# Optimization experiments

Hardware: AMD Instinct MI355X
Metric: run time of the kernel (lower is better)

The kernel has to match this reference:

```python
import jax, jax.numpy as jnp
import numpy as np
from jax import lax

K_GROUPS = 4
CH = 256
CG = CH // K_GROUPS  # 64
KK = 9  # 3x3 kernel taps


def setup_inputs() -> dict:
    key = jax.random.key(0)
    ks = jax.random.split(key, 4)
    x = jax.random.normal(ks[0], (16, CH, 64, 64), dtype=jnp.float32)
    # offset-predicting conv: Cg -> 18 (2 offsets per 3x3 tap); small init so offsets are modest
    off_w = jax.random.normal(ks[1], (K_GROUPS, 18, CG, 3, 3), dtype=jnp.float32) * 0.01
    off_b = jnp.zeros((K_GROUPS, 18), dtype=jnp.float32)
    # deformable conv weights: Cg -> Cg, 3x3
    def_w = jax.random.normal(ks[2], (K_GROUPS, CG, CG, 3, 3), dtype=jnp.float32) * (1.0 / np.sqrt(CG * KK))
    def_b = jnp.zeros((K_GROUPS, CG), dtype=jnp.float32)
    return {"x": x, "off_w": off_w, "off_b": off_b, "def_w": def_w, "def_b": def_b}


def _bilinear_sample(img, py, px):
    # img: [B,Cg,H,W]; py,px: [B,KK,H,W] float sample coords -> [B,Cg,KK,H,W]
    B, C, H, W = img.shape
    K = py.shape[1]
    imgf = img.reshape(B, C, H * W)
    y0 = jnp.floor(py)
    x0 = jnp.floor(px)
    wy = py - y0
    wx = px - x0

    def gather(yi, xi, wgt):
        valid = (yi >= 0) & (yi < H) & (xi >= 0) & (xi < W)  # zero padding outside
        yc = jnp.clip(yi, 0, H - 1).astype(jnp.int32)
        xc = jnp.clip(xi, 0, W - 1).astype(jnp.int32)
        idx = (yc * W + xc).reshape(B, 1, K * H * W)
        v = jnp.take_along_axis(imgf, idx, axis=2).reshape(B, C, K, H, W)
        w = (wgt * valid.astype(img.dtype)).reshape(B, 1, K, H, W)
        return v * w

    return (gather(y0, x0, (1 - wy) * (1 - wx))
            + gather(y0, x0 + 1, (1 - wy) * wx)
            + gather(y0 + 1, x0, wy * (1 - wx))
            + gather(y0 + 1, x0 + 1, wy * wx))


def _group_forward(xg, ow, ob, dw, db):
    # xg: [B,Cg,H,W]
    B, C, H, W = xg.shape
    offset = lax.conv_general_dilated(xg, ow, (1, 1), ((1, 1), (1, 1)),
                                      dimension_numbers=("NCHW", "OIHW", "NCHW"))
    offset = offset + ob[None, :, None, None]            # [B,18,H,W]
    off = offset.reshape(B, KK, 2, H, W)                  # per-tap (dy,dx)
    ky, kx = jnp.meshgrid(jnp.arange(-1, 2), jnp.arange(-1, 2), indexing="ij")
    ky = ky.reshape(KK).astype(xg.dtype)
    kx = kx.reshape(KK).astype(xg.dtype)
    hh = jnp.arange(H, dtype=xg.dtype)
    ww = jnp.arange(W, dtype=xg.dtype)
    py = off[:, :, 0] + ky[None, :, None, None] + hh[None, None, :, None]  # [B,KK,H,W]
    px = off[:, :, 1] + kx[None, :, None, None] + ww[None, None, None, :]
    sampled = _bilinear_sample(xg, py, px)                # [B,Cg,KK,H,W]
    out = jnp.einsum("oik,bikhw->bohw", dw.reshape(dw.shape[0], dw.shape[1], KK), sampled)
    return out + db[None, :, None, None]


def reference(x, off_w, off_b, def_w, def_b):
    xs = jnp.split(x, K_GROUPS, axis=1)  # mirrors torch.split over channel groups
    outs = [_group_forward(xs[g], off_w[g], off_b[g], def_w[g], def_b[g])
            for g in range(K_GROUPS)]
    return jnp.concatenate(outs, axis=1)
```

## Files before the change

kernel.cpp:

```cpp
#include <hip/hip_runtime.h>
#include <hip/hip_bf16.h>
#include <hip/hip_fp16.h>

#define B_  16
#define G_  4
#define CG  64
#define H_  64
#define W_  64
#define KK  9
#define HW  (H_ * W_)
#define IP  72
#define PD  68
#define XSLICE (PD * PD * CG)

typedef short    short8  __attribute__((ext_vector_type(8)));
typedef _Float16 half8   __attribute__((ext_vector_type(8)));
typedef _Float16 h2      __attribute__((ext_vector_type(2)));
typedef float    f32x4   __attribute__((ext_vector_type(4)));
typedef float    f32x16  __attribute__((ext_vector_type(16)));

__device__ __forceinline__ short f2h(float v) {
    _Float16 h = (_Float16)v;
    short s;
    __builtin_memcpy(&s, &h, 2);
    return s;
}

__device__ __forceinline__ unsigned int pk2h(float a, float b) {
    h2 h = { (_Float16)a, (_Float16)b };
    unsigned int u;
    __builtin_memcpy(&u, &h, 4);
    return u;
}

__device__ __forceinline__ unsigned int interp2h(unsigned int c00, unsigned int c01,
                                                 unsigned int c10, unsigned int c11,
                                                 h2 w00, h2 w01, h2 w10, h2 w11) {
    h2 v00, v01, v10, v11;
    __builtin_memcpy(&v00, &c00, 4);
    __builtin_memcpy(&v01, &c01, 4);
    __builtin_memcpy(&v10, &c10, 4);
    __builtin_memcpy(&v11, &c11, 4);
    h2 r = v00 * w00 + v01 * w01 + v10 * w10 + v11 * w11;
    unsigned int o;
    __builtin_memcpy(&o, &r, 4);
    return o;
}

__global__ __launch_bounds__(256)
void prep_all(const float* __restrict__ x,
              const float* __restrict__ off_w,
              const float* __restrict__ def_w,
              short* __restrict__ xTpad,
              short* __restrict__ dwA32,
              short* __restrict__ owA)
{
    const int blk = blockIdx.x;
    const int t   = threadIdx.x;

    if (blk < 1024) {
        const int bg = blk >> 4;
        const int y0 = (blk & 15) * 4;

        __shared__ unsigned int sBw[4 * CG * 33];

        const float* src = x + (size_t)bg * CG * HW + (size_t)y0 * W_;
        const int i  = t >> 2;
        const int x0 = (t & 3) * 16;

        float4 v[4][4];
#pragma unroll
        for (int r = 0; r < 4; r++) {
            const float* sp = src + (size_t)i * HW + r * W_ + x0;
#pragma unroll
            for (int c = 0; c < 4; c++) v[r][c] = ((const float4*)sp)[c];
        }

#pragma unroll
        for (int r = 0; r < 4; r++) {
#pragma unroll
            for (int c = 0; c < 4; c++) {
                const unsigned int u0 = pk2h(v[r][c].x, v[r][c].y);
                const unsigned int u1 = pk2h(v[r][c].z, v[r][c].w);
                const int base = (r * CG + i) * 33 + ((x0 + 4 * c) >> 1);
                sBw[base]     = u0;
                sBw[base + 1] = u1;
            }
        }
        __syncthreads();

        const short* sBs = (const short*)sBw;
        short* dst = xTpad + (size_t)bg * XSLICE;
#pragma unroll
        for (int r = 0; r < 4; r++) {
            const int yp = y0 + 2 + r;
            for (int task = t; task < PD * 8; task += 256) {
                const int ich = task & 7;
                const int xp  = task >> 3;
                const int xx  = xp - 2;
                short8 o = {0, 0, 0, 0, 0, 0, 0, 0};
                if ((unsigned)xx < (unsigned)W_) {
#pragma unroll
                    for (int e = 0; e < 8; e++)
                        o[e] = sBs[(r * CG + ich * 8 + e) * 66 + xx];
                }
                *(short8*)(dst + ((size_t)yp * PD + xp) * CG + ich * 8) = o;
            }
        }
        return;
    }

    if (blk < 1088) {
        const int bg = blk - 1024;
        short* dstb = xTpad + (size_t)bg * XSLICE;
        const int4 z = {0, 0, 0, 0};
        int4* d0 = (int4*)(dstb);
        int4* d1 = (int4*)(dstb + (size_t)66 * PD * CG);
        const int n16 = (2 * PD * CG * 2) / 16;
        for (int c = t; c < n16; c += 256) { d0[c] = z; d1[c] = z; }
        return;
    }

    const int tid = (blk - 1088) * 256 + t;
    const int ndw = G_ * KK * 4096;
    const int now = G_ * 18 * 2 * 4 * 16 * 8;
    if (tid < ndw) {
        const int e    = tid & 7;
        const int o    = (tid >> 3) & 31;
        const int q2   = (tid >> 8) & 1;
        const int step = (tid >> 9) & 3;
        const int mt   = (tid >> 11) & 1;
        const int gk   = tid >> 12;
        const int k    = gk % KK;
        const int g    = gk / KK;
        const int oo   = mt * 32 + o;
        const int i    = step * 16 + q2 * 8 + e;
        dwA32[tid] = f2h(def_w[((g * CG + oo) * CG + i) * KK + k]);
    } else if (tid < ndw + now) {
        const int t2 = tid - ndw;
        const int e  = t2 & 7;
        const int jj = (t2 >> 3) & 15;
        const int q  = (t2 >> 7) & 3;
        const int tm = (t2 >> 9) & 1;
        const int gs = t2 >> 10;
        const int s  = gs % 18;
        const int g  = gs / 18;
        const int j  = tm * 16 + jj;
        const int rc = s >> 1;
        const int i  = (s & 1) * 32 + q * 8 + e;
        owA[t2] = (j < 18) ? f2h(off_w[((g * 18 + j) * CG + i) * KK + rc]) : (short)0;
    }
}

__global__ __launch_bounds__(256, 7)
void deform_main(const short* __restrict__ xTpad,
                 const float* __restrict__ off_b,
                 const float* __restrict__ def_b,
                 const short* __restrict__ dwA32,
                 const short* __restrict__ owA,
                 float* __restrict__ out)
{
    const int raw = blockIdx.x;
    const int r8  = raw & 7;
    const int h   = (raw >> 3) & 63;
    const int q8  = raw >> 9;
    const int bg  = q8 * 8 + r8;
    const int b   = bg >> 2;
    const int g   = bg & 3;

    __shared__ float2 pcs[KK][64];
    __shared__ short  sT[2][64 * IP];

    const int t    = threadIdx.x;
    const int lane = t & 63;
    const int p    = t >> 6;
    const int nn   = lane & 15;
    const int q    = lane >> 4;

    const short* xb = xTpad + (size_t)bg * XSLICE;

    {
        const short* owAg = owA + g * 18 * 1024;
        f32x4 oa0 = {0.f, 0.f, 0.f, 0.f};
        f32x4 oa1 = {0.f, 0.f, 0.f, 0.f};
#pragma unroll
        for (int rc = 0; rc < 9; rc++) {
            const int rr = rc / 3;
            const int cc = rc % 3;
            const short* cp = xb + ((h + rr + 1) * PD + (p * 16 + nn + cc + 1)) * CG + q * 8;
            const half8 b0 = *(const half8*)cp;
            const half8 b1 = *(const half8*)(cp + 32);
            const int s0 = rc * 2, s1 = rc * 2 + 1;
            const half8 a00 = *(const half8*)(owAg + ((s0 * 2 + 0) * 4 + q) * 128 + nn * 8);
            const half8 a01 = *(const half8*)(owAg + ((s0 * 2 + 1) * 4 + q) * 128 + nn * 8);
            const half8 a10 = *(const half8*)(owAg + ((s1 * 2 + 0) * 4 + q) * 128 + nn * 8);
            const half8 a11 = *(const half8*)(owAg + ((s1 * 2 + 1) * 4 + q) * 128 + nn * 8);
            oa0 = __builtin_amdgcn_mfma_f32_16x16x32_f16(a00, b0, oa0, 0, 0, 0);
            oa1 = __builtin_amdgcn_mfma_f32_16x16x32_f16(a01, b0, oa1, 0, 0, 0);
            oa0 = __builtin_amdgcn_mfma_f32_16x16x32_f16(a10, b1, oa0, 0, 0, 0);
            oa1 = __builtin_amdgcn_mfma_f32_16x16x32_f16(a11, b1, oa1, 0, 0, 0);
        }
        const int n = p * 16 + nn;
#pragma unroll
        for (int reg = 0; reg < 4; reg++) {
            const int j  = q * 4 + reg;
            const int kk = j >> 1;
            const float v = oa0[reg] + off_b[g * 18 + j];
            if ((j & 1) == 0) pcs[kk][n].x = v + (float)(kk / 3) + (float)(h + 1);
            else              pcs[kk][n].y = v + (float)(kk % 3) + (float)(n + 1);
        }
        if (q == 0) {
            pcs[8][n].x = oa1[0] + off_b[g * 18 + 16] + 2.0f + (float)(h + 1);
            pcs[8][n].y = oa1[1] + off_b[g * 18 + 17] + 2.0f + (float)(n + 1);
        }
    }

    const int mt  = p >> 1;
    const int nt  = p & 1;
    const int n31 = lane & 31;
    const int q2  = lane >> 5;

    f32x16 acc = {0.f};
    const short* dwg = dwA32 + g * KK * 4096;

    const int posL  = lane >> 3;
    const int chidx = lane & 7;

    auto gather_tap = [&](int k, short* __restrict__ sTb) {
#pragma unroll
        for (int it = 0; it < 2; it++) {
            const int pos = p * 16 + it * 8 + posL;
            const float2 pc = pcs[k][pos];
            const float yf = floorf(pc.x);
            const float xf = floorf(pc.y);
            const float wy = pc.x - yf;
            const float wx = pc.y - xf;
            int y0 = (int)yf;
            int x0 = (int)xf;
            y0 = (y0 < 0) ? 0 : ((y0 > 66) ? 66 : y0);
            x0 = (x0 < 0) ? 0 : ((x0 > 66) ? 66 : x0);
            const short* cp = xb + (y0 * PD + x0) * CG + chidx * 8;
            const uint4 c00 = *(const uint4*)cp;
            const uint4 c01 = *(const uint4*)(cp + CG);
            const uint4 c10 = *(const uint4*)(cp + PD * CG);
            const uint4 c11 = *(const uint4*)(cp + PD * CG + CG);
            const float a00 = (1.0f - wy) * (1.0f - wx);
            const float a01 = (1.0f - wy) * wx;
            const float a10 = wy * (1.0f - wx);
            const float a11 = wy * wx;
            const h2 w00 = { (_Float16)a00, (_Float16)a00 };
            const h2 w01 = { (_Float16)a01, (_Float16)a01 };
            const h2 w10 = { (_Float16)a10, (_Float16)a10 };
            const h2 w11 = { (_Float16)a11, (_Float16)a11 };
            uint4 ov;
            ov.x = interp2h(c00.x, c01.x, c10.x, c11.x, w00, w01, w10, w11);
            ov.y = interp2h(c00.y, c01.y, c10.y, c11.y, w00, w01, w10, w11);
            ov.z = interp2h(c00.z, c01.z, c10.z, c11.z, w00, w01, w10, w11);
            ov.w = interp2h(c00.w, c01.w, c10.w, c11.w, w00, w01, w10, w11);
            *(uint4*)&sTb[pos * IP + chidx * 8] = ov;
        }
    };

    auto einsum_tap = [&](int k, const short* __restrict__ sTb) {
        const short* dwk = dwg + k * 4096;
#pragma unroll
        for (int step = 0; step < 4; step++) {
            const half8 af = *(const half8*)(dwk + ((mt * 4 + step) * 2 + q2) * 256 + n31 * 8);
            const half8 bf = *(const half8*)&sTb[(nt * 32 + n31) * IP + step * 16 + q2 * 8];
            acc = __builtin_amdgcn_mfma_f32_32x32x16_f16(af, bf, acc, 0, 0, 0);
        }
    };

    gather_tap(0, &sT[0][0]);
    __syncthreads();
    for (int k = 0; k < KK; k++) {
        if (k < KK - 1) gather_tap(k + 1, &sT[(k + 1) & 1][0]);
        einsum_tap(k, &sT[k & 1][0]);
        __syncthreads();
    }

    float* outb = out + (size_t)(b * 256 + g * 64) * HW + h * W_;
    const int n = nt * 32 + n31;
#pragma unroll
    for (int reg = 0; reg < 16; reg++) {
        const int o = mt * 32 + (reg & 3) + 8 * (reg >> 2) + 4 * q2;
        outb[(size_t)o * HW + n] = acc[reg] + def_b[g * 64 + o];
    }
}

__global__ __launch_bounds__(256, 4)
void deform_fallback(const float* __restrict__ x,
                     const float* __restrict__ off_w,
                     const float* __restrict__ off_b,
                     const float* __restrict__ def_w,
                     const float* __restrict__ def_b,
                     float* __restrict__ out)
{
    const int raw = blockIdx.x;
    const int r8  = raw & 7;
    const int h   = (raw >> 3) & 63;
    const int q8  = raw >> 9;
    const int bg  = q8 * 8 + r8;
    const int b   = bg >> 2;
    const int g   = bg & 3;

    __shared__ float pys[KK][W_];
    __shared__ float pxs[KK][W_];
    __shared__ float buf[8192];
    float* red   = buf;
    float* s_lds = buf;
    float* dwTl  = buf + 4096;

    const int t = threadIdx.x;
    const int w = t & 63;
    const int p = t >> 6;

    const float* xg = x + (size_t)(b * 256 + g * 64) * HW;

    float acc[18];
#pragma unroll
    for (int j = 0; j < 18; j++) acc[j] = 0.0f;
    {
        const int i0 = p * 16;
        for (int ii = 0; ii < 16; ii++) {
            const int i = i0 + ii;
            const float* xi = xg + i * HW;
#pragma unroll
            for (int r = 0; r < 3; r++) {
                const int y = h + r - 1;
                if ((unsigned)y >= (unsigned)H_) continue;
#pragma unroll
                for (int c = 0; c < 3; c++) {
                    const int xc = w + c - 1;
                    const float xv = ((unsigned)xc < (unsigned)W_) ? xi[y * W_ + xc] : 0.0f;
#pragma unroll
                    for (int j = 0; j < 18; j++) {
                        const float wv = off_w[((g * 18 + j) * CG + i) * 9 + r * 3 + c];
                        acc[j] = fmaf(wv, xv, acc[j]);
                    }
                }
            }
        }
    }
#pragma unroll
    for (int j = 0; j < 18; j++) red[(p * 18 + j) * 64 + w] = acc[j];
    __syncthreads();
    for (int idx = t; idx < 18 * 64; idx += 256) {
        const int j  = idx >> 6;
        const int ww = idx & 63;
        float v = red[(0 * 18 + j) * 64 + ww] + red[(1 * 18 + j) * 64 + ww]
                + red[(2 * 18 + j) * 64 + ww] + red[(3 * 18 + j) * 64 + ww];
        v += off_b[g * 18 + j];
        const int k = j >> 1;
        if ((j & 1) == 0) pys[k][ww] = v + (float)(k / 3 - 1) + (float)h;
        else              pxs[k][ww] = v + (float)(k % 3 - 1) + (float)ww;
    }
    __syncthreads();

    float facc[16];
#pragma unroll
    for (int qd = 0; qd < 16; qd++) facc[qd] = 0.0f;
    const int w4 = (t & 15) << 2;
    const int o4 = (t >> 4) << 2;

    for (int k = 0; k < KK; k++) {
#pragma unroll
        for (int n = 0; n < 16; n++) {
            const int v = t + 256 * n;
            const int i = v >> 6;
            const int o = v & 63;
            dwTl[v] = def_w[((g * CG + o) * CG + i) * KK + k];
        }
        const float py  = pys[k][w];
        const float px  = pxs[k][w];
        const float y0f = floorf(py);
        const float x0f = floorf(px);
        const float wy  = py - y0f;
        const float wx  = px - x0f;
        const int   y0  = (int)y0f;
        const int   x0  = (int)x0f;
        const float w00 = (1.0f - wy) * (1.0f - wx);
        const float w01 = (1.0f - wy) * wx;
        const float w10 = wy * (1.0f - wx);
        const float w11 = wy * wx;
        const bool vy0 = (unsigned)y0       < (unsigned)H_;
        const bool vy1 = (unsigned)(y0 + 1) < (unsigned)H_;
        const bool vx0 = (unsigned)x0       < (unsigned)W_;
        const bool vx1 = (unsigned)(x0 + 1) < (unsigned)W_;
        const int a00 = y0 * W_ + x0;
#pragma unroll
        for (int n = 0; n < 16; n++) {
            const int i = (n << 2) + p;
            const float* xi = xg + i * HW;
            const float v00 = (vy0 && vx0) ? xi[a00]          : 0.0f;
            const float v01 = (vy0 && vx1) ? xi[a00 + 1]      : 0.0f;
            const float v10 = (vy1 && vx0) ? xi[a00 + W_]     : 0.0f;
            const float v11 = (vy1 && vx1) ? xi[a00 + W_ + 1] : 0.0f;
            s_lds[i * 64 + w] = w00 * v00 + w01 * v01 + w10 * v10 + w11 * v11;
        }
        __syncthreads();
#pragma unroll 4
        for (int i = 0; i < CG; i++) {
            const float4 sv = *(const float4*)&s_lds[i * 64 + w4];
            const float4 dv = *(const float4*)&dwTl[i * 64 + o4];
            facc[0]  = fmaf(dv.x, sv.x, facc[0]);
            facc[1]  = fmaf(dv.x, sv.y, facc[1]);
            facc[2]  = fmaf(dv.x, sv.z, facc[2]);
            facc[3]  = fmaf(dv.x, sv.w, facc[3]);
            facc[4]  = fmaf(dv.y, sv.x, facc[4]);
            facc[5]  = fmaf(dv.y, sv.y, facc[5]);
            facc[6]  = fmaf(dv.y, sv.z, facc[6]);
            facc[7]  = fmaf(dv.y, sv.w, facc[7]);
            facc[8]  = fmaf(dv.z, sv.x, facc[8]);
            facc[9]  = fmaf(dv.z, sv.y, facc[9]);
            facc[10] = fmaf(dv.z, sv.z, facc[10]);
            facc[11] = fmaf(dv.z, sv.w, facc[11]);
            facc[12] = fmaf(dv.w, sv.x, facc[12]);
            facc[13] = fmaf(dv.w, sv.y, facc[13]);
            facc[14] = fmaf(dv.w, sv.z, facc[14]);
            facc[15] = fmaf(dv.w, sv.w, facc[15]);
        }
        __syncthreads();
    }

    float* outp = out + (size_t)(b * 256 + g * 64) * HW + h * W_;
#pragma unroll
    for (int oo = 0; oo < 4; oo++) {
        const int o = o4 + oo;
        const float bias = def_b[g * 64 + o];
        float4 r;
        r.x = facc[oo * 4 + 0] + bias;
        r.y = facc[oo * 4 + 1] + bias;
        r.z = facc[oo * 4 + 2] + bias;
        r.w = facc[oo * 4 + 3] + bias;
        *(float4*)&outp[o * HW + w4] = r;
    }
}

extern "C" void kernel_launch(void* const* d_in, const int* in_sizes, int n_in,
                              void* d_out, int out_size, void* d_ws, size_t ws_size,
                              hipStream_t stream)
{
    (void)in_sizes; (void)n_in; (void)out_size;
    const float* x     = (const float*)d_in[0];
    const float* off_w = (const float*)d_in[1];
    const float* off_b = (const float*)d_in[2];
    const float* def_w = (const float*)d_in[3];
    const float* def_b = (const float*)d_in[4];
    float* out = (float*)d_out;

    const size_t xT_bytes  = (size_t)B_ * G_ * XSLICE * 2;
    const size_t dw_bytes  = (size_t)G_ * KK * 4096 * 2;
    const size_t ow_bytes  = (size_t)G_ * 18 * 1024 * 2;
    const size_t need = xT_bytes + dw_bytes + ow_bytes;

    const int nblk   = B_ * G_ * H_;
    const int nprepw = (G_ * KK * 4096 + G_ * 18 * 1024 + 255) / 256;
    const int nprep  = 1024 + 64 + nprepw;

    if (ws_size >= need) {
        short* xTpad = (short*)d_ws;
        short* dwA32 = (short*)((char*)d_ws + xT_bytes);
        short* owA   = (short*)((char*)d_ws + xT_bytes + dw_bytes);
        prep_all<<<nprep, 256, 0, stream>>>(x, off_w, def_w, xTpad, dwA32, owA);
        deform_main<<<nblk, 256, 0, stream>>>(xTpad, off_b, def_b, dwA32, owA, out);
    } else {
        deform_fallback<<<nblk, 256, 0, stream>>>(x, off_w, off_b, def_w, def_b, out);
    }
}
```

Baseline: 221.0 us.

## Make each wave own its pixel slice to drop block barriers in tap loop

Restructures the einsum so each wave computes all 64 output channels for its own 16 pixels with 16x16x32 MFMAs, instead of 32x32 tiles that share gathered data across waves. Each wave therefore only reads the samples it gathered itself, so the per-tap __syncthreads are removed and every wave gets private double-buffered LDS. Gather loads are split into issue and write phases kept in registers, so the next tap's global loads overlap the current MFMAs. The def_w prep layout changes to match, and launch bounds drop from 7 to 5 blocks per CU to make room for the extra registers, which lowers occupancy.

```diff
diff --git a/kernel.cpp b/kernel.cpp
--- a/kernel.cpp
+++ b/kernel.cpp
@@ -52,7 +52,7 @@
               const float* __restrict__ off_w,
               const float* __restrict__ def_w,
               short* __restrict__ xTpad,
-              short* __restrict__ dwA32,
+              short* __restrict__ dwA16,
               short* __restrict__ owA)
 {
     const int blk = blockIdx.x;
@@ -125,17 +125,16 @@
     const int ndw = G_ * KK * 4096;
     const int now = G_ * 18 * 2 * 4 * 16 * 8;
     if (tid < ndw) {
-        const int e    = tid & 7;
-        const int o    = (tid >> 3) & 31;
-        const int q2   = (tid >> 8) & 1;
-        const int step = (tid >> 9) & 3;
-        const int mt   = (tid >> 11) & 1;
-        const int gk   = tid >> 12;
-        const int k    = gk % KK;
-        const int g    = gk / KK;
-        const int oo   = mt * 32 + o;
-        const int i    = step * 16 + q2 * 8 + e;
-        dwA32[tid] = f2h(def_w[((g * CG + oo) * CG + i) * KK + k]);
+        const int e  = tid & 7;
+        const int l  = (tid >> 3) & 63;
+        const int kh = (tid >> 9) & 1;
+        const int ot = (tid >> 10) & 3;
+        const int gk = tid >> 12;
+        const int k  = gk % KK;
+        const int g  = gk / KK;
+        const int o  = ot * 16 + (l & 15);
+        const int i  = kh * 32 + (l >> 4) * 8 + e;
+        dwA16[tid] = f2h(def_w[((g * CG + o) * CG + i) * KK + k]);
     } else if (tid < ndw + now) {
         const int t2 = tid - ndw;
         const int e  = t2 & 7;
@@ -152,11 +151,11 @@
     }
 }
 
-__global__ __launch_bounds__(256, 7)
+__global__ __launch_bounds__(256, 5)
 void deform_main(const short* __restrict__ xTpad,
                  const float* __restrict__ off_b,
                  const float* __restrict__ def_b,
-                 const short* __restrict__ dwA32,
+                 const short* __restrict__ dwA16,
                  const short* __restrict__ owA,
                  float* __restrict__ out)
 {
@@ -169,7 +168,7 @@
     const int g   = bg & 3;
 
     __shared__ float2 pcs[KK][64];
-    __shared__ short  sT[2][64 * IP];
+    __shared__ short  sT[4][2][16 * IP];
 
     const int t    = threadIdx.x;
     const int lane = t & 63;
@@ -215,35 +214,40 @@
         }
     }
 
-    const int mt  = p >> 1;
-    const int nt  = p & 1;
-    const int n31 = lane & 31;
-    const int q2  = lane >> 5;
-
-    f32x16 acc = {0.f};
-    const short* dwg = dwA32 + g * KK * 4096;
-
     const int posL  = lane >> 3;
     const int chidx = lane & 7;
 
-    auto gather_tap = [&](int k, short* __restrict__ sTb) {
+    short* sW0 = &sT[p][0][0];
+    short* sW1 = &sT[p][1][0];
+
+    f32x4 acc[4] = { {0.f}, {0.f}, {0.f}, {0.f} };
+    const short* dwg = dwA16 + g * KK * 4096;
+
+    auto issue_tap = [&](int k, uint4* cr, float2* wv) {
 #pragma unroll
         for (int it = 0; it < 2; it++) {
             const int pos = p * 16 + it * 8 + posL;
             const float2 pc = pcs[k][pos];
             const float yf = floorf(pc.x);
             const float xf = floorf(pc.y);
-            const float wy = pc.x - yf;
-            const float wx = pc.y - xf;
+            wv[it] = make_float2(pc.x - yf, pc.y - xf);
             int y0 = (int)yf;
             int x0 = (int)xf;
             y0 = (y0 < 0) ? 0 : ((y0 > 66) ? 66 : y0);
             x0 = (x0 < 0) ? 0 : ((x0 > 66) ? 66 : x0);
             const short* cp = xb + (y0 * PD + x0) * CG + chidx * 8;
-            const uint4 c00 = *(const uint4*)cp;
-            const uint4 c01 = *(const uint4*)(cp + CG);
-            const uint4 c10 = *(const uint4*)(cp + PD * CG);
-            const uint4 c11 = *(const uint4*)(cp + PD * CG + CG);
+            cr[it * 4 + 0] = *(const uint4*)cp;
+            cr[it * 4 + 1] = *(const uint4*)(cp + CG);
+            cr[it * 4 + 2] = *(const uint4*)(cp + PD * CG);
+            cr[it * 4 + 3] = *(const uint4*)(cp + PD * CG + CG);
+        }
+    };
+
+    auto write_tap = [&](short* __restrict__ sTb, const uint4* cr, const float2* wv) {
+#pragma unroll
+        for (int it = 0; it < 2; it++) {
+            const float wy = wv[it].x;
+            const float wx = wv[it].y;
             const float a00 = (1.0f - wy) * (1.0f - wx);
             const float a01 = (1.0f - wy) * wx;
             const float a10 = wy * (1.0f - wx);
@@ -252,39 +256,57 @@
             const h2 w01 = { (_Float16)a01, (_Float16)a01 };
             const h2 w10 = { (_Float16)a10, (_Float16)a10 };
             const h2 w11 = { (_Float16)a11, (_Float16)a11 };
+            const uint4 c00 = cr[it * 4 + 0];
+            const uint4 c01 = cr[it * 4 + 1];
+            const uint4 c10 = cr[it * 4 + 2];
+            const uint4 c11 = cr[it * 4 + 3];
             uint4 ov;
             ov.x = interp2h(c00.x, c01.x, c10.x, c11.x, w00, w01, w10, w11);
             ov.y = interp2h(c00.y, c01.y, c10.y, c11.y, w00, w01, w10, w11);
             ov.z = interp2h(c00.z, c01.z, c10.z, c11.z, w00, w01, w10, w11);
             ov.w = interp2h(c00.w, c01.w, c10.w, c11.w, w00, w01, w10, w11);
-            *(uint4*)&sTb[pos * IP + chidx * 8] = ov;
+            *(uint4*)&sTb[(it * 8 + posL) * IP + chidx * 8] = ov;
         }
     };
 
     auto einsum_tap = [&](int k, const short* __restrict__ sTb) {
         const short* dwk = dwg + k * 4096;
 #pragma unroll
-        for (int step = 0; step < 4; step++) {
-            const half8 af = *(const half8*)(dwk + ((mt * 4 + step) * 2 + q2) * 256 + n31 * 8);
-            const half8 bf = *(const half8*)&sTb[(nt * 32 + n31) * IP + step * 16 + q2 * 8];
-            acc = __builtin_amdgcn_mfma_f32_32x32x16_f16(af, bf, acc, 0, 0, 0);
+        for (int kh = 0; kh < 2; kh++) {
+            const half8 bf = *(const half8*)&sTb[nn * IP + kh * 32 + q * 8];
+#pragma unroll
+            for (int ot = 0; ot < 4; ot++) {
+                const half8 af = *(const half8*)(dwk + ((ot * 2 + kh) * 64 + lane) * 8);
+                acc[ot] = __builtin_amdgcn_mfma_f32_16x16x32_f16(af, bf, acc[ot], 0, 0, 0);
+            }
         }
     };
 
-    gather_tap(0, &sT[0][0]);
-    __syncthreads();
+    uint4  crA[8], crB[8];
+    float2 wvA[2], wvB[2];
+
+    issue_tap(0, crA, wvA);
+    write_tap(sW0, crA, wvA);
+#pragma unroll
     for (int k = 0; k < KK; k++) {
-        if (k < KK - 1) gather_tap(k + 1, &sT[(k + 1) & 1][0]);
-        einsum_tap(k, &sT[k & 1][0]);
-        __syncthreads();
+        short*  bufCur = ((k & 1) == 0) ? sW0 : sW1;
+        short*  bufNxt = ((k & 1) == 0) ? sW1 : sW0;
+        uint4*  crN    = ((k & 1) == 0) ? crB : crA;
+        float2* wvN    = ((k & 1) == 0) ? wvB : wvA;
+        if (k < KK - 1) issue_tap(k + 1, crN, wvN);
+        einsum_tap(k, bufCur);
+        if (k < KK - 1) write_tap(bufNxt, crN, wvN);
     }
 
     float* outb = out + (size_t)(b * 256 + g * 64) * HW + h * W_;
-    const int n = nt * 32 + n31;
-#pragma unroll
-    for (int reg = 0; reg < 16; reg++) {
-        const int o = mt * 32 + (reg & 3) + 8 * (reg >> 2) + 4 * q2;
-        outb[(size_t)o * HW + n] = acc[reg] + def_b[g * 64 + o];
+    const int n = p * 16 + nn;
+#pragma unroll
+    for (int ot = 0; ot < 4; ot++) {
+#pragma unroll
+        for (int reg = 0; reg < 4; reg++) {
+            const int o = ot * 16 + q * 4 + reg;
+            outb[(size_t)o * HW + n] = acc[ot][reg] + def_b[g * 64 + o];
+        }
     }
 }
 
@@ -460,10 +482,10 @@
 
     if (ws_size >= need) {
         short* xTpad = (short*)d_ws;
-        short* dwA32 = (short*)((char*)d_ws + xT_bytes);
+        short* dwA16 = (short*)((char*)d_ws + xT_bytes);
         short* owA   = (short*)((char*)d_ws + xT_bytes + dw_bytes);
-        prep_all<<<nprep, 256, 0, stream>>>(x, off_w, def_w, xTpad, dwA32, owA);
-        deform_main<<<nblk, 256, 0, stream>>>(xTpad, off_b, def_b, dwA32, owA, out);
+        prep_all<<<nprep, 256, 0, stream>>>(x, off_w, def_w, xTpad, dwA16, owA);
+        deform_main<<<nblk, 256, 0, stream>>>(xTpad, off_b, def_b, dwA16, owA, out);
     } else {
         deform_fallback<<<nblk, 256, 0, stream>>>(x, off_w, off_b, def_w, def_b, out);
     }
```

After: 234.6 us. 1.06x slower.

## Stage 5-row input window in XOR-swizzled LDS for offset conv and gather

Applied to the files above, without the earlier changes.

Each block now loads a 5-row by 66-column window of the padded fp16 input into shared memory, with an XOR swizzle to avoid bank conflicts. The offset-prediction conv reads its B operands from this window, and the bilinear gather reads its four corners from it when the sample falls inside. Out-of-window samples still read from global memory. The extra LDS footprint (about 42 KB) leads to lowering launch_bounds occupancy from 7 to 2. This trades global/L2 traffic for lower occupancy and a load phase followed by a barrier.

```diff
diff --git a/kernel.cpp b/kernel.cpp
--- a/kernel.cpp
+++ b/kernel.cpp
@@ -12,6 +12,11 @@
 #define IP  72
 #define PD  68
 #define XSLICE (PD * PD * CG)
+
+#define WROWS 5
+#define WCOLS 66
+#define NCELL (WROWS * WCOLS)
+#define NSLOT (NCELL * 8)
 
 typedef short    short8  __attribute__((ext_vector_type(8)));
 typedef _Float16 half8   __attribute__((ext_vector_type(8)));
@@ -152,7 +157,7 @@
     }
 }
 
-__global__ __launch_bounds__(256, 7)
+__global__ __launch_bounds__(256, 2)
 void deform_main(const short* __restrict__ xTpad,
                  const float* __restrict__ off_b,
                  const float* __restrict__ def_b,
@@ -168,6 +173,7 @@
     const int b   = bg >> 2;
     const int g   = bg & 3;
 
+    __shared__ short  sX[NSLOT * 8];
     __shared__ float2 pcs[KK][64];
     __shared__ short  sT[2][64 * IP];
 
@@ -180,6 +186,32 @@
     const short* xb = xTpad + (size_t)bg * XSLICE;
 
     {
+        uint4 tmp[10];
+#pragma unroll
+        for (int j = 0; j < 10; j++) {
+            const int s    = j * 256 + t;
+            const int cell = s >> 3;
+            const int c    = (s & 7) ^ (cell & 7);
+            const int rr   = cell / WCOLS;
+            const int colx = 1 + (cell - rr * WCOLS);
+            tmp[j] = *(const uint4*)(xb + ((h + rr) * PD + colx) * CG + c * 8);
+        }
+        uint4 tl;
+        const int st = 2560 + t;
+        if (t < NSLOT - 2560) {
+            const int cell = st >> 3;
+            const int c    = (st & 7) ^ (cell & 7);
+            const int rr   = cell / WCOLS;
+            const int colx = 1 + (cell - rr * WCOLS);
+            tl = *(const uint4*)(xb + ((h + rr) * PD + colx) * CG + c * 8);
+        }
+#pragma unroll
+        for (int j = 0; j < 10; j++) *(uint4*)&sX[(j * 256 + t) * 8] = tmp[j];
+        if (t < NSLOT - 2560) *(uint4*)&sX[st * 8] = tl;
+    }
+    __syncthreads();
+
+    {
         const short* owAg = owA + g * 18 * 1024;
         f32x4 oa0 = {0.f, 0.f, 0.f, 0.f};
         f32x4 oa1 = {0.f, 0.f, 0.f, 0.f};
@@ -187,9 +219,10 @@
         for (int rc = 0; rc < 9; rc++) {
             const int rr = rc / 3;
             const int cc = rc % 3;
-            const short* cp = xb + ((h + rr + 1) * PD + (p * 16 + nn + cc + 1)) * CG + q * 8;
-            const half8 b0 = *(const half8*)cp;
-            const half8 b1 = *(const half8*)(cp + 32);
+            const int cA   = p * 16 + nn + cc + 1;
+            const int cell = (rr + 1) * WCOLS + (cA - 1);
+            const half8 b0 = *(const half8*)&sX[(cell * 8 + ( q      ^ (cell & 7))) * 8];
+            const half8 b1 = *(const half8*)&sX[(cell * 8 + ((q + 4) ^ (cell & 7))) * 8];
             const int s0 = rc * 2, s1 = rc * 2 + 1;
             const half8 a00 = *(const half8*)(owAg + ((s0 * 2 + 0) * 4 + q) * 128 + nn * 8);
             const half8 a01 = *(const half8*)(owAg + ((s0 * 2 + 1) * 4 + q) * 128 + nn * 8);
@@ -239,15 +272,32 @@
             int x0 = (int)xf;
             y0 = (y0 < 0) ? 0 : ((y0 > 66) ? 66 : y0);
             x0 = (x0 < 0) ? 0 : ((x0 > 66) ? 66 : x0);
-            const short* cp = xb + (y0 * PD + x0) * CG + chidx * 8;
-            const uint4 c00 = *(const uint4*)cp;
-            const uint4 c01 = *(const uint4*)(cp + CG);
-            const uint4 c10 = *(const uint4*)(cp + PD * CG);
-            const uint4 c11 = *(const uint4*)(cp + PD * CG + CG);
-            const float a00 = (1.0f - wy) * (1.0f - wx);
-            const float a01 = (1.0f - wy) * wx;
-            const float a10 = wy * (1.0f - wx);
-            const float a11 = wy * wx;
+            float a00 = (1.0f - wy) * (1.0f - wx);
+            float a01 = (1.0f - wy) * wx;
+            float a10 = wy * (1.0f - wx);
+            float a11 = wy * wx;
+            uint4 c00, c01, c10, c11;
+            const int ry = y0 - h;
+            if (ry >= 0 && ry <= WROWS - 2) {
+                int col0 = x0 - 1;
+                int col1 = x0;
+                if (col0 < 0)          { a00 = 0.f; a10 = 0.f; col0 = 0; }
+                if (col1 > WCOLS - 1)  { a01 = 0.f; a11 = 0.f; col1 = WCOLS - 1; }
+                const int ca = ry * WCOLS + col0;
+                const int cb = ry * WCOLS + col1;
+                const int cc_ = ca + WCOLS;
+                const int cd = cb + WCOLS;
+                c00 = *(const uint4*)&sX[(ca  * 8 + (chidx ^ (ca  & 7))) * 8];
+                c01 = *(const uint4*)&sX[(cb  * 8 + (chidx ^ (cb  & 7))) * 8];
+                c10 = *(const uint4*)&sX[(cc_ * 8 + (chidx ^ (cc_ & 7))) * 8];
+                c11 = *(const uint4*)&sX[(cd  * 8 + (chidx ^ (cd  & 7))) * 8];
+            } else {
+                const short* cp = xb + (y0 * PD + x0) * CG + chidx * 8;
+                c00 = *(const uint4*)cp;
+                c01 = *(const uint4*)(cp + CG);
+                c10 = *(const uint4*)(cp + PD * CG);
+                c11 = *(const uint4*)(cp + PD * CG + CG);
+            }
             const h2 w00 = { (_Float16)a00, (_Float16)a00 };
             const h2 w01 = { (_Float16)a01, (_Float16)a01 };
             const h2 w10 = { (_Float16)a10, (_Float16)a10 };
```

After: 232.9 us. 1.05x slower.

## Stage a 5-row input window in LDS and gather bilinear taps from it

Applied to the files above, without the earlier changes.

Each block now loads a 5x68-cell fp16 window of the padded input into shared memory. Both the offset-conv fragments and the bilinear corner reads come from LDS whenever the sample row falls inside the window, with a global-memory fallback otherwise. The double-buffered sT pipeline is replaced by a single buffer with two barriers per tap, and the next tap's deformable weights are prefetched into registers. The much larger LDS footprint (about 54KB) and the lower launch-bounds occupancy target (7 to 2 blocks) trade latency hiding for on-chip reuse.

```diff
diff --git a/kernel.cpp b/kernel.cpp
--- a/kernel.cpp
+++ b/kernel.cpp
@@ -12,6 +12,11 @@
 #define IP  72
 #define PD  68
 #define XSLICE (PD * PD * CG)
+
+#define WR   5
+#define WC   68
+#define CELLW 72
+#define NSLOT (WR * WC * 8)
 
 typedef short    short8  __attribute__((ext_vector_type(8)));
 typedef _Float16 half8   __attribute__((ext_vector_type(8)));
@@ -152,7 +157,7 @@
     }
 }
 
-__global__ __launch_bounds__(256, 7)
+__global__ __launch_bounds__(256, 2)
 void deform_main(const short* __restrict__ xTpad,
                  const float* __restrict__ off_b,
                  const float* __restrict__ def_b,
@@ -168,8 +173,9 @@
     const int b   = bg >> 2;
     const int g   = bg & 3;
 
+    __shared__ short  sX[WR * WC * CELLW];
+    __shared__ short  sT[64 * IP];
     __shared__ float2 pcs[KK][64];
-    __shared__ short  sT[2][64 * IP];
 
     const int t    = threadIdx.x;
     const int lane = t & 63;
@@ -180,6 +186,40 @@
     const short* xb = xTpad + (size_t)bg * XSLICE;
 
     {
+        uint4 tv[10];
+#pragma unroll
+        for (int j = 0; j < 10; j++) {
+            const int s    = j * 256 + t;
+            const int cell = s >> 3;
+            const int ch   = s & 7;
+            const int r    = cell / WC;
+            const int c    = cell - r * WC;
+            tv[j] = *(const uint4*)(xb + ((h + r) * PD + c) * CG + ch * 8);
+        }
+        uint4 tl;
+        if (t < NSLOT - 2560) {
+            const int s    = 2560 + t;
+            const int cell = s >> 3;
+            const int ch   = s & 7;
+            const int r    = cell / WC;
+            const int c    = cell - r * WC;
+            tl = *(const uint4*)(xb + ((h + r) * PD + c) * CG + ch * 8);
+        }
+#pragma unroll
+        for (int j = 0; j < 10; j++) {
+            const int s    = j * 256 + t;
+            const int cell = s >> 3;
+            const int ch   = s & 7;
+            *(uint4*)&sX[cell * CELLW + ch * 8] = tv[j];
+        }
+        if (t < NSLOT - 2560) {
+            const int s    = 2560 + t;
+            *(uint4*)&sX[(s >> 3) * CELLW + (s & 7) * 8] = tl;
+        }
+    }
+    __syncthreads();
+
+    {
         const short* owAg = owA + g * 18 * 1024;
         f32x4 oa0 = {0.f, 0.f, 0.f, 0.f};
         f32x4 oa1 = {0.f, 0.f, 0.f, 0.f};
@@ -187,9 +227,10 @@
         for (int rc = 0; rc < 9; rc++) {
             const int rr = rc / 3;
             const int cc = rc % 3;
-            const short* cp = xb + ((h + rr + 1) * PD + (p * 16 + nn + cc + 1)) * CG + q * 8;
-            const half8 b0 = *(const half8*)cp;
-            const half8 b1 = *(const half8*)(cp + 32);
+            const int cA   = p * 16 + nn + cc + 1;
+            const int cell = (rr + 1) * WC + cA;
+            const half8 b0 = *(const half8*)&sX[cell * CELLW + q * 8];
+            const half8 b1 = *(const half8*)&sX[cell * CELLW + (q + 4) * 8];
             const int s0 = rc * 2, s1 = rc * 2 + 1;
             const half8 a00 = *(const half8*)(owAg + ((s0 * 2 + 0) * 4 + q) * 128 + nn * 8);
             const half8 a01 = *(const half8*)(owAg + ((s0 * 2 + 1) * 4 + q) * 128 + nn * 8);
@@ -226,7 +267,7 @@
     const int posL  = lane >> 3;
     const int chidx = lane & 7;
 
-    auto gather_tap = [&](int k, short* __restrict__ sTb) {
+    auto gather_tap = [&](int k) {
 #pragma unroll
         for (int it = 0; it < 2; it++) {
             const int pos = p * 16 + it * 8 + posL;
@@ -239,11 +280,21 @@
             int x0 = (int)xf;
             y0 = (y0 < 0) ? 0 : ((y0 > 66) ? 66 : y0);
             x0 = (x0 < 0) ? 0 : ((x0 > 66) ? 66 : x0);
-            const short* cp = xb + (y0 * PD + x0) * CG + chidx * 8;
-            const uint4 c00 = *(const uint4*)cp;
-            const uint4 c01 = *(const uint4*)(cp + CG);
-            const uint4 c10 = *(const uint4*)(cp + PD * CG);
-            const uint4 c11 = *(const uint4*)(cp + PD * CG + CG);
+            uint4 c00, c01, c10, c11;
+            const int ry = y0 - h;
+            if ((unsigned)ry <= 3u) {
+                const int base = (ry * WC + x0) * CELLW + chidx * 8;
+                c00 = *(const uint4*)&sX[base];
+                c01 = *(const uint4*)&sX[base + CELLW];
+                c10 = *(const uint4*)&sX[base + WC * CELLW];
+                c11 = *(const uint4*)&sX[base + WC * CELLW + CELLW];
+            } else {
+                const short* cp = xb + (y0 * PD + x0) * CG + chidx * 8;
+                c00 = *(const uint4*)cp;
+                c01 = *(const uint4*)(cp + CG);
+                c10 = *(const uint4*)(cp + PD * CG);
+                c11 = *(const uint4*)(cp + PD * CG + CG);
+            }
             const float a00 = (1.0f - wy) * (1.0f - wx);
             const float a01 = (1.0f - wy) * wx;
             const float a10 = wy * (1.0f - wx);
@@ -257,25 +308,38 @@
             ov.y = interp2h(c00.y, c01.y, c10.y, c11.y, w00, w01, w10, w11);
             ov.z = interp2h(c00.z, c01.z, c10.z, c11.z, w00, w01, w10, w11);
             ov.w = interp2h(c00.w, c01.w, c10.w, c11.w, w00, w01, w10, w11);
-            *(uint4*)&sTb[pos * IP + chidx * 8] = ov;
+            *(uint4*)&sT[pos * IP + chidx * 8] = ov;
         }
     };
 
-    auto einsum_tap = [&](int k, const short* __restrict__ sTb) {
-        const short* dwk = dwg + k * 4096;
-#pragma unroll
-        for (int step = 0; step < 4; step++) {
-            const half8 af = *(const half8*)(dwk + ((mt * 4 + step) * 2 + q2) * 256 + n31 * 8);
-            const half8 bf = *(const half8*)&sTb[(nt * 32 + n31) * IP + step * 16 + q2 * 8];
-            acc = __builtin_amdgcn_mfma_f32_32x32x16_f16(af, bf, acc, 0, 0, 0);
-        }
-    };
-
-    gather_tap(0, &sT[0][0]);
-    __syncthreads();
+    half8 af0, af1, af2, af3, an0, an1, an2, an3;
+    {
+        const short* dwk = dwg;
+        af0 = *(const half8*)(dwk + ((mt * 4 + 0) * 2 + q2) * 256 + n31 * 8);
+        af1 = *(const half8*)(dwk + ((mt * 4 + 1) * 2 + q2) * 256 + n31 * 8);
+        af2 = *(const half8*)(dwk + ((mt * 4 + 2) * 2 + q2) * 256 + n31 * 8);
+        af3 = *(const half8*)(dwk + ((mt * 4 + 3) * 2 + q2) * 256 + n31 * 8);
+    }
+
     for (int k = 0; k < KK; k++) {
-        if (k < KK - 1) gather_tap(k + 1, &sT[(k + 1) & 1][0]);
-        einsum_tap(k, &sT[k & 1][0]);
+        gather_tap(k);
+        __syncthreads();
+        if (k < KK - 1) {
+            const short* dwk = dwg + (k + 1) * 4096;
+            an0 = *(const half8*)(dwk + ((mt * 4 + 0) * 2 + q2) * 256 + n31 * 8);
+            an1 = *(const half8*)(dwk + ((mt * 4 + 1) * 2 + q2) * 256 + n31 * 8);
+            an2 = *(const half8*)(dwk + ((mt * 4 + 2) * 2 + q2) * 256 + n31 * 8);
+            an3 = *(const half8*)(dwk + ((mt * 4 + 3) * 2 + q2) * 256 + n31 * 8);
+        }
+        const half8 bf0 = *(const half8*)&sT[(nt * 32 + n31) * IP + 0 * 16 + q2 * 8];
+        const half8 bf1 = *(const half8*)&sT[(nt * 32 + n31) * IP + 1 * 16 + q2 * 8];
+        const half8 bf2 = *(const half8*)&sT[(nt * 32 + n31) * IP + 2 * 16 + q2 * 8];
+        const half8 bf3 = *(const half8*)&sT[(nt * 32 + n31) * IP + 3 * 16 + q2 * 8];
+        acc = __builtin_amdgcn_mfma_f32_32x32x16_f16(af0, bf0, acc, 0, 0, 0);
+        acc = __builtin_amdgcn_mfma_f32_32x32x16_f16(af1, bf1, acc, 0, 0, 0);
+        acc = __builtin_amdgcn_mfma_f32_32x32x16_f16(af2, bf2, acc, 0, 0, 0);
+        acc = __builtin_amdgcn_mfma_f32_32x32x16_f16(af3, bf3, acc, 0, 0, 0);
+        if (k < KK - 1) { af0 = an0; af1 = an1; af2 = an2; af3 = an3; }
         __syncthreads();
     }
 
```

After: 225.5 us. 1.02x slower.
